# Kernel optimization log

Hardware: AMD Instinct MI355X
Metric: run time of the kernel (lower is better)

## Reference

```python
import jax, jax.numpy as jnp
import numpy as np

D_MODEL = 1024
N_HEADS = 16
D_K = D_MODEL // N_HEADS
D_FF = 4096
B, S = 2, 2048
EPS = 1e-5
SCALE = 0.02


def setup_inputs() -> dict:
    key = jax.random.key(0)
    ks = jax.random.split(key, 8)
    return {
        "x": jax.random.normal(ks[0], (B, S, D_MODEL), dtype=jnp.float32),
        "ln1_w": jnp.ones((D_MODEL,), jnp.float32),
        "ln1_b": jnp.zeros((D_MODEL,), jnp.float32),
        "Wq": jax.random.normal(ks[1], (D_MODEL, D_MODEL), jnp.float32) * SCALE,
        "bq": jnp.zeros((D_MODEL,), jnp.float32),
        "Wk": jax.random.normal(ks[2], (D_MODEL, D_MODEL), jnp.float32) * SCALE,
        "bk": jnp.zeros((D_MODEL,), jnp.float32),
        "Wv": jax.random.normal(ks[3], (D_MODEL, D_MODEL), jnp.float32) * SCALE,
        "bv": jnp.zeros((D_MODEL,), jnp.float32),
        "Wo": jax.random.normal(ks[4], (D_MODEL, D_MODEL), jnp.float32) * SCALE,
        "bo": jnp.zeros((D_MODEL,), jnp.float32),
        "ln2_w": jnp.ones((D_MODEL,), jnp.float32),
        "ln2_b": jnp.zeros((D_MODEL,), jnp.float32),
        "W1": jax.random.normal(ks[5], (D_MODEL, D_FF), jnp.float32) * SCALE,
        "b1": jnp.zeros((D_FF,), jnp.float32),
        "W2": jax.random.normal(ks[6], (D_FF, D_MODEL), jnp.float32) * SCALE,
        "b2": jnp.zeros((D_MODEL,), jnp.float32),
    }


def _layernorm(x, w, b):
    mu = jnp.mean(x, axis=-1, keepdims=True)
    var = jnp.mean(jnp.square(x - mu), axis=-1, keepdims=True)
    return (x - mu) * jax.lax.rsqrt(var + EPS) * w + b


def reference(x, ln1_w, ln1_b, Wq, bq, Wk, bk, Wv, bv, Wo, bo,
              ln2_w, ln2_b, W1, b1, W2, b2):
    # Pre-norm multi-head self-attention (dropout = identity, eval mode)
    h = _layernorm(x, ln1_w, ln1_b)                      # [B,S,D]
    q = (h @ Wq + bq).reshape(B, S, N_HEADS, D_K)        # [B,S,H,Dk]
    k = (h @ Wk + bk).reshape(B, S, N_HEADS, D_K)
    v = (h @ Wv + bv).reshape(B, S, N_HEADS, D_K)
    scores = jnp.einsum('bqhd,bkhd->bhqk', q, k) / jnp.sqrt(jnp.float32(D_K))
    attn = jax.nn.softmax(scores, axis=-1)               # [B,H,S,S]
    ctx = jnp.einsum('bhqk,bkhd->bqhd', attn, v).reshape(B, S, D_MODEL)
    x = x + (ctx @ Wo + bo)
    # Pre-norm FFN
    h2 = _layernorm(x, ln2_w, ln2_b)
    ff = jax.nn.relu(h2 @ W1 + b1) @ W2 + b2
    return x + ff
```

## Files before the change

kernel.cpp:

```cpp
#include <hip/hip_runtime.h>
#include <hip/hip_bf16.h>
#include <cstdint>
#include <cstddef>

typedef unsigned short ushort_t;
typedef __bf16 bf16x8 __attribute__((ext_vector_type(8)));
typedef float f32x4 __attribute__((ext_vector_type(4)));

#define D_MODEL 1024
#define D_FF 4096
#define BB 2
#define SS 2048
#define NH 16
#define MROWS (BB * SS)
#define KVBLK 64

__device__ __forceinline__ ushort_t f2bf(float f) {
  union { float f; unsigned u; } x; x.f = f;
  unsigned r = x.u + 0x7fffu + ((x.u >> 16) & 1u);
  return (ushort_t)(r >> 16);
}

__device__ __forceinline__ void gload_lds16(const void* g, void* l) {
  __builtin_amdgcn_global_load_lds((const __attribute__((address_space(1))) void*)g,
                                   (__attribute__((address_space(3))) void*)l, 16, 0, 0);
}

__device__ __forceinline__ float dpp_sum16(float x) {
  int v;
  v = __builtin_amdgcn_update_dpp(0, __float_as_int(x), 0xB1, 0xF, 0xF, true);
  x += __int_as_float(v);
  v = __builtin_amdgcn_update_dpp(0, __float_as_int(x), 0x4E, 0xF, 0xF, true);
  x += __int_as_float(v);
  v = __builtin_amdgcn_update_dpp(0, __float_as_int(x), 0x141, 0xF, 0xF, true);
  x += __int_as_float(v);
  v = __builtin_amdgcn_update_dpp(0, __float_as_int(x), 0x140, 0xF, 0xF, true);
  x += __int_as_float(v);
  return x;
}

__global__ __launch_bounds__(256) void ln_bf16_kernel(
    const float* __restrict__ x, const float* __restrict__ w,
    const float* __restrict__ b, ushort_t* __restrict__ out) {
  int row = blockIdx.x;
  int tid = threadIdx.x;
  int lane = tid & 63, wid = tid >> 6;
  const float4 v = ((const float4*)(x + (size_t)row * D_MODEL))[tid];
  float s = v.x + v.y + v.z + v.w;
  __shared__ float red[8];
  #pragma unroll
  for (int o = 32; o > 0; o >>= 1) s += __shfl_down(s, o);
  if (lane == 0) red[wid] = s;
  __syncthreads();
  float mu = (red[0] + red[1] + red[2] + red[3]) * (1.0f / D_MODEL);
  float d0 = v.x - mu, d1 = v.y - mu, d2 = v.z - mu, d3 = v.w - mu;
  float sq = d0 * d0 + d1 * d1 + d2 * d2 + d3 * d3;
  #pragma unroll
  for (int o = 32; o > 0; o >>= 1) sq += __shfl_down(sq, o);
  if (lane == 0) red[4 + wid] = sq;
  __syncthreads();
  float var = (red[4] + red[5] + red[6] + red[7]) * (1.0f / D_MODEL);
  float rstd = rsqrtf(var + 1e-5f);
  const float4 wv = ((const float4*)w)[tid];
  const float4 bv = ((const float4*)b)[tid];
  ushort4 o4;
  o4.x = f2bf(d0 * rstd * wv.x + bv.x);
  o4.y = f2bf(d1 * rstd * wv.y + bv.y);
  o4.z = f2bf(d2 * rstd * wv.z + bv.z);
  o4.w = f2bf(d3 * rstd * wv.w + bv.w);
  ((ushort4*)(out + (size_t)row * D_MODEL))[tid] = o4;
}

__global__ __launch_bounds__(256) void transpose_cast_kernel(
    const float* __restrict__ W, ushort_t* __restrict__ Wt, int K, int N) {
  __shared__ float tile[32][33];
  int bx = blockIdx.x * 32;
  int by = blockIdx.y * 32;
  int tx = threadIdx.x, ty = threadIdx.y;
  #pragma unroll
  for (int i = 0; i < 32; i += 8)
    tile[ty + i][tx] = W[(size_t)(by + ty + i) * N + bx + tx];
  __syncthreads();
  #pragma unroll
  for (int i = 0; i < 32; i += 8)
    Wt[(size_t)(bx + ty + i) * K + by + tx] = f2bf(tile[tx][ty + i]);
}

__global__ __launch_bounds__(256) void vtrans_kernel(
    const ushort_t* __restrict__ qkv, ushort_t* __restrict__ Vt) {
  __shared__ __align__(16) ushort_t T[64 * 64];
  const int tid = threadIdx.x;
  const int bh = blockIdx.y, b = bh >> 4, h = bh & 15;
  const int kv0 = blockIdx.x * 64;
  const ushort_t* Vp = qkv + (size_t)b * SS * 3072 + 2048 + h * 64;
  #pragma unroll
  for (int i = 0; i < 2; i++) {
    int idx = tid * 2 + i;
    int key = idx >> 3, c = idx & 7;
    bf16x8 v = *(const bf16x8*)(Vp + (size_t)(kv0 + key) * 3072 + c * 8);
    *(bf16x8*)(T + key * 64 + ((c ^ (key & 7)) * 8)) = v;
  }
  __syncthreads();
  int d = tid >> 2, kb = tid & 3;
  ushort_t o[16];
  #pragma unroll
  for (int j = 0; j < 16; j++) {
    int key = kb * 16 + j;
    o[j] = T[key * 64 + (((d >> 3) ^ (key & 7)) * 8) + (d & 7)];
  }
  ushort_t* dst = Vt + (size_t)(bh * 64 + d) * SS + kv0 + kb * 16;
  *(bf16x8*)dst = *(bf16x8*)&o[0];
  *(bf16x8*)(dst + 8) = *(bf16x8*)&o[8];
}

template <int EPI>
__global__ __launch_bounds__(256, 2) void gemm128_kernel(
    const ushort_t* __restrict__ A, const ushort_t* __restrict__ Bt,
    const float* __restrict__ bias, const float* __restrict__ resid,
    void* __restrict__ Cout, int M, int N, int K, int NTn) {
  __shared__ __align__(16) ushort_t lds[4][2][4096];
  const int tid = threadIdx.x, lane = tid & 63, wid = tid >> 6;
  const int wm = wid >> 1, wn = wid & 1;
  const int rl = lane & 15, cg = lane >> 4;
  int nwg = gridDim.x;
  int q = nwg >> 3, rr = nwg & 7;
  int xcd = blockIdx.x & 7, idx = blockIdx.x >> 3;
  int wgid = (xcd < rr ? xcd * (q + 1) : rr * (q + 1) + (xcd - rr) * q) + idx;
  const int row0 = (wgid / NTn) * 128, col0 = (wgid - (wgid / NTn) * NTn) * 128;
  const int NT = K / 32;

  int soff[2], ldso[2];
  #pragma unroll
  for (int i = 0; i < 2; i++) {
    int ci = wid * 128 + i * 64 + lane;
    int P = ci * 16;
    int L = P ^ (((P >> 7) & 7) << 4);
    int row = L >> 6, kc = (L >> 4) & 3;
    soff[i] = row * K + kc * 8;
    ldso[i] = (wid * 128 + i * 64) * 8;
  }

  f32x4 acc[4][4] = {};

  auto stage = [&](int t) {
    int b = t & 3;
    int kk = t * 32;
    #pragma unroll
    for (int i = 0; i < 2; i++) {
      gload_lds16(A + (size_t)row0 * K + kk + soff[i], &lds[b][0][ldso[i]]);
      gload_lds16(Bt + (size_t)col0 * K + kk + soff[i], &lds[b][1][ldso[i]]);
    }
  };

  auto compute = [&](int t) {
    int b = t & 3;
    bf16x8 af[4], bfv[4];
    #pragma unroll
    for (int mi = 0; mi < 4; mi++) {
      int r = wm * 64 + mi * 16 + rl;
      int L = r * 64 + cg * 16;
      int P = L ^ (((L >> 7) & 7) << 4);
      af[mi] = *(const bf16x8*)&lds[b][0][P >> 1];
    }
    #pragma unroll
    for (int ni = 0; ni < 4; ni++) {
      int r = wn * 64 + ni * 16 + rl;
      int L = r * 64 + cg * 16;
      int P = L ^ (((L >> 7) & 7) << 4);
      bfv[ni] = *(const bf16x8*)&lds[b][1][P >> 1];
    }
    __builtin_amdgcn_s_setprio(1);
    #pragma unroll
    for (int mi = 0; mi < 4; mi++)
      #pragma unroll
      for (int ni = 0; ni < 4; ni++)
        acc[mi][ni] = __builtin_amdgcn_mfma_f32_16x16x32_bf16(af[mi], bfv[ni], acc[mi][ni], 0, 0, 0);
    __builtin_amdgcn_s_setprio(0);
  };

  stage(0); stage(1); stage(2);
  for (int t = 0; t < NT; ++t) {
    if (t < NT - 2)       asm volatile("s_waitcnt vmcnt(8)" ::: "memory");
    else if (t == NT - 2) asm volatile("s_waitcnt vmcnt(4)" ::: "memory");
    else                  asm volatile("s_waitcnt vmcnt(0)" ::: "memory");
    __builtin_amdgcn_s_barrier();
    __builtin_amdgcn_sched_barrier(0);
    if (t + 3 < NT) stage(t + 3);
    compute(t);
  }

  if (EPI == 2) {
    float* out = (float*)Cout;
    #pragma unroll
    for (int ni = 0; ni < 4; ni++) {
      int col = col0 + wn * 64 + ni * 16 + rl;
      float bv = bias[col];
      #pragma unroll
      for (int mi = 0; mi < 4; mi++) {
        int rowb = row0 + wm * 64 + mi * 16 + cg * 4;
        #pragma unroll
        for (int j = 0; j < 4; j++)
          out[(size_t)(rowb + j) * N + col] =
              acc[mi][ni][j] + bv + resid[(size_t)(rowb + j) * N + col];
      }
    }
  } else {
    ushort_t* out = (ushort_t*)Cout;
    #pragma unroll
    for (int ni = 0; ni < 4; ni++) {
      int col = col0 + wn * 64 + ni * 16 + rl;
      float bv = bias[col];
      float sc = (EPI == 0 && col < 1024) ? 0.18033688011f : 1.0f;
      #pragma unroll
      for (int mi = 0; mi < 4; mi++) {
        int rowb = row0 + wm * 64 + mi * 16 + cg * 4;
        #pragma unroll
        for (int j = 0; j < 4; j++) {
          float v = acc[mi][ni][j] + bv;
          if (EPI == 1) v = fmaxf(v, 0.0f);
          if (EPI == 0) v *= sc;
          out[(size_t)(rowb + j) * N + col] = f2bf(v);
        }
      }
    }
  }
}

__global__ __launch_bounds__(256) void attn_kernel(
    const ushort_t* __restrict__ qkv, const ushort_t* __restrict__ Vt,
    ushort_t* __restrict__ ctx) {
  __shared__ __align__(16) ushort_t Kl[2][64 * 64];
  __shared__ __align__(16) ushort_t Vl[2][64 * 64];
  __shared__ __align__(16) ushort_t Pl[4][16 * 64];
  const int tid = threadIdx.x, lane = tid & 63, wid = tid >> 6;
  int bid = blockIdx.y * 32 + blockIdx.x;
  int w = (bid & 7) * 128 + (bid >> 3);
  const int bh = w >> 5, qt = w & 31;
  const int b = bh >> 4, h = bh & 15;
  const int q0 = qt * 64 + wid * 16;
  const ushort_t* Qp = qkv + (size_t)b * SS * 3072 + h * 64;
  const ushort_t* Kp = Qp + 1024;
  const ushort_t* Vg = Vt + (size_t)bh * 64 * SS;

  bf16x8 qf[2];
  {
    int qr = q0 + (lane & 15);
    #pragma unroll
    for (int s2 = 0; s2 < 2; s2++)
      qf[s2] = *(const bf16x8*)(Qp + (size_t)qr * 3072 + s2 * 32 + (lane >> 4) * 8);
  }
  float l[4];
  f32x4 acc[4] = {};
  #pragma unroll
  for (int r = 0; r < 4; r++) l[r] = 0.f;

  const int NT = SS / KVBLK;

  int ksrc[2], vsrc[2];
  #pragma unroll
  for (int i = 0; i < 2; i++) {
    int idx = wid * 128 + i * 64 + lane;
    int R = idx >> 3, c = idx & 7;
    int key = (R & 15) * 4 + (R >> 4);
    ksrc[i] = key * 3072 + ((c ^ (R & 7)) * 8);
    vsrc[i] = R * SS + ((c ^ (R & 7)) * 8);
  }
  const int ldsb = wid * 1024;

  auto stageKV = [&](int buf, int t) {
    size_t kvK = (size_t)t * KVBLK * 3072;
    int kvV = t * KVBLK;
    gload_lds16(Kp + kvK + ksrc[0], &Kl[buf][ldsb]);
    gload_lds16(Kp + kvK + ksrc[1], &Kl[buf][ldsb + 512]);
    gload_lds16(Vg + kvV + vsrc[0], &Vl[buf][ldsb]);
    gload_lds16(Vg + kvV + vsrc[1], &Vl[buf][ldsb + 512]);
  };

  auto body = [&](int t, int cb) {
    __syncthreads();
    if (t + 1 < NT) stageKV(cb ^ 1, t + 1);

    f32x4 s4[4] = {};
    #pragma unroll
    for (int g = 0; g < 4; g++) {
      const ushort_t* kr = &Kl[cb][(g * 16 + (lane & 15)) * 64];
      bf16x8 kf0 = *(const bf16x8*)(kr + (((lane >> 4)) ^ ((lane & 15) & 7)) * 8);
      bf16x8 kf1 = *(const bf16x8*)(kr + ((4 + (lane >> 4)) ^ ((lane & 15) & 7)) * 8);
      s4[g] = __builtin_amdgcn_mfma_f32_16x16x32_bf16(qf[0], kf0, s4[g], 0, 0, 0);
      s4[g] = __builtin_amdgcn_mfma_f32_16x16x32_bf16(qf[1], kf1, s4[g], 0, 0, 0);
    }
    const int qrow = (lane >> 4) * 4;
    const int cp = (lane & 15) >> 1, hf = (lane & 15) & 1;
    #pragma unroll
    for (int r = 0; r < 4; r++) {
      float p0 = __builtin_amdgcn_exp2f(s4[0][r]);
      float p1 = __builtin_amdgcn_exp2f(s4[1][r]);
      float p2 = __builtin_amdgcn_exp2f(s4[2][r]);
      float p3 = __builtin_amdgcn_exp2f(s4[3][r]);
      l[r] += (p0 + p1) + (p2 + p3);
      unsigned w0, w1;
      asm("v_cvt_pk_bf16_f32 %0, %1, %2" : "=v"(w0) : "v"(p0), "v"(p1));
      asm("v_cvt_pk_bf16_f32 %0, %1, %2" : "=v"(w1) : "v"(p2), "v"(p3));
      uint2 pw; pw.x = w0; pw.y = w1;
      int qq = qrow + r;
      *(uint2*)(&Pl[wid][qq * 64 + ((cp ^ (qq & 7)) * 8) + hf * 4]) = pw;
    }
    asm volatile("s_waitcnt lgkmcnt(0)" ::: "memory");
    __builtin_amdgcn_sched_barrier(0);
    bf16x8 pf[2];
    {
      int qq = lane & 15;
      #pragma unroll
      for (int ks = 0; ks < 2; ks++) {
        int c = ks * 4 + (lane >> 4);
        pf[ks] = *(const bf16x8*)(&Pl[wid][qq * 64 + ((c ^ (qq & 7)) * 8)]);
      }
    }
    #pragma unroll
    for (int f = 0; f < 4; f++) {
      int d = f * 16 + (lane & 15);
      #pragma unroll
      for (int ks = 0; ks < 2; ks++) {
        int chunk = (ks * 4 + (lane >> 4)) ^ (d & 7);
        bf16x8 vf = *(const bf16x8*)(&Vl[cb][d * 64 + chunk * 8]);
        acc[f] = __builtin_amdgcn_mfma_f32_16x16x32_bf16(pf[ks], vf, acc[f], 0, 0, 0);
      }
    }
  };

  stageKV(0, 0);
  for (int t = 0; t < NT; t += 2) {
    body(t, 0);
    body(t + 1, 1);
  }

  #pragma unroll
  for (int r = 0; r < 4; r++) l[r] = dpp_sum16(l[r]);
  float rl4[4];
  #pragma unroll
  for (int r = 0; r < 4; r++) rl4[r] = 1.0f / l[r];
  #pragma unroll
  for (int f = 0; f < 4; f++)
    #pragma unroll
    for (int r = 0; r < 4; r++) {
      int row = b * SS + q0 + (lane >> 4) * 4 + r;
      int col = h * 64 + f * 16 + (lane & 15);
      ctx[(size_t)row * D_MODEL + col] = f2bf(acc[f][r] * rl4[r]);
    }
}

extern "C" void kernel_launch(void* const* d_in, const int* in_sizes, int n_in,
                              void* d_out, int out_size, void* d_ws, size_t ws_size,
                              hipStream_t stream) {
  const float* x    = (const float*)d_in[0];
  const float* ln1w = (const float*)d_in[1];
  const float* ln1b = (const float*)d_in[2];
  const float* Wq   = (const float*)d_in[3];
  const float* bq   = (const float*)d_in[4];
  const float* Wk   = (const float*)d_in[5];
  const float* bk   = (const float*)d_in[6];
  const float* Wv   = (const float*)d_in[7];
  const float* bv   = (const float*)d_in[8];
  const float* Wo   = (const float*)d_in[9];
  const float* bo   = (const float*)d_in[10];
  const float* ln2w = (const float*)d_in[11];
  const float* ln2b = (const float*)d_in[12];
  const float* W1   = (const float*)d_in[13];
  const float* b1   = (const float*)d_in[14];
  const float* W2   = (const float*)d_in[15];
  const float* b2   = (const float*)d_in[16];

  char* ws = (char*)d_ws;
  size_t off = 0;
  auto alloc = [&](size_t bytes) {
    void* p = ws + off;
    off += (bytes + 255) & ~(size_t)255;
    return p;
  };
  ushort_t* Wt_qkv = (ushort_t*)alloc((size_t)3072 * 1024 * 2);
  ushort_t* Wt_o   = (ushort_t*)alloc((size_t)1024 * 1024 * 2);
  ushort_t* Wt_1   = (ushort_t*)alloc((size_t)4096 * 1024 * 2);
  ushort_t* Wt_2   = (ushort_t*)alloc((size_t)1024 * 4096 * 2);
  float*    bqkv   = (float*)alloc((size_t)3072 * 4);
  ushort_t* qkvb   = (ushort_t*)alloc((size_t)MROWS * 3072 * 2);
  ushort_t* ctxb   = (ushort_t*)alloc((size_t)MROWS * 1024 * 2);
  ushort_t* hbuf   = (ushort_t*)alloc((size_t)MROWS * 1024 * 2);
  float*    x2     = (float*)alloc((size_t)MROWS * 1024 * 4);
  ushort_t* Vtb    = (ushort_t*)alloc((size_t)BB * NH * 64 * SS * 2);
  ushort_t* ff1    = qkvb;
  float*    outp   = (float*)d_out;

  dim3 tb(32, 8);
  transpose_cast_kernel<<<dim3(32, 32), tb, 0, stream>>>(Wq, Wt_qkv, 1024, 1024);
  transpose_cast_kernel<<<dim3(32, 32), tb, 0, stream>>>(Wk, Wt_qkv + 1024 * 1024, 1024, 1024);
  transpose_cast_kernel<<<dim3(32, 32), tb, 0, stream>>>(Wv, Wt_qkv + 2 * 1024 * 1024, 1024, 1024);
  transpose_cast_kernel<<<dim3(32, 32), tb, 0, stream>>>(Wo, Wt_o, 1024, 1024);
  transpose_cast_kernel<<<dim3(128, 32), tb, 0, stream>>>(W1, Wt_1, 1024, 4096);
  transpose_cast_kernel<<<dim3(32, 128), tb, 0, stream>>>(W2, Wt_2, 4096, 1024);
  hipMemcpyAsync(bqkv,        bq, 1024 * 4, hipMemcpyDeviceToDevice, stream);
  hipMemcpyAsync(bqkv + 1024, bk, 1024 * 4, hipMemcpyDeviceToDevice, stream);
  hipMemcpyAsync(bqkv + 2048, bv, 1024 * 4, hipMemcpyDeviceToDevice, stream);

  ln_bf16_kernel<<<MROWS, 256, 0, stream>>>(x, ln1w, ln1b, hbuf);
  gemm128_kernel<0><<<dim3(24 * 32), 256, 0, stream>>>(
      hbuf, Wt_qkv, bqkv, nullptr, qkvb, MROWS, 3072, 1024, 24);
  vtrans_kernel<<<dim3(SS / 64, BB * NH), 256, 0, stream>>>(qkvb, Vtb);
  attn_kernel<<<dim3(SS / 64, BB * NH), 256, 0, stream>>>(qkvb, Vtb, ctxb);
  gemm128_kernel<2><<<dim3(8 * 32), 256, 0, stream>>>(
      ctxb, Wt_o, bo, x, x2, MROWS, 1024, 1024, 8);
  ln_bf16_kernel<<<MROWS, 256, 0, stream>>>(x2, ln2w, ln2b, hbuf);
  gemm128_kernel<1><<<dim3(32 * 32), 256, 0, stream>>>(
      hbuf, Wt_1, b1, nullptr, ff1, MROWS, D_FF, 1024, 32);
  gemm128_kernel<2><<<dim3(8 * 32), 256, 0, stream>>>(
      ff1, Wt_2, b2, x2, outp, MROWS, 1024, 4096, 8);
}
```

Baseline: 254.6 us.

## Add 64x128-tile GEMM kernel for N=1024 residual projections to fill more CUs

Adds a gemm64_kernel that uses 64x128 output tiles, 3-stage LDS buffering and an XCD-aware workgroup remap. It replaces the 128x128 gemm for the Wo and W2 projections (the N=1024 outputs with fp32 residual epilogue). This doubles the workgroup count from 256 to 512, giving better occupancy across the MI355X CUs. The cost is more redundant B-tile loads and smaller per-wave MFMA reuse.

Result: slower. 269.6 us (+5.9%).

```diff
diff --git a/kernel.cpp b/kernel.cpp
--- a/kernel.cpp
+++ b/kernel.cpp
@@ -189,39 +189,116 @@
     compute(t);
   }
 
-  if (EPI == 2) {
-    float* out = (float*)Cout;
+  ushort_t* out = (ushort_t*)Cout;
+  #pragma unroll
+  for (int ni = 0; ni < 4; ni++) {
+    int col = col0 + wn * 64 + ni * 16 + rl;
+    float bv = bias[col];
+    float sc = (EPI == 0 && col < 1024) ? 0.18033688011f : 1.0f;
+    #pragma unroll
+    for (int mi = 0; mi < 4; mi++) {
+      int rowb = row0 + wm * 64 + mi * 16 + cg * 4;
+      #pragma unroll
+      for (int j = 0; j < 4; j++) {
+        float v = acc[mi][ni][j] + bv;
+        if (EPI == 1) v = fmaxf(v, 0.0f);
+        if (EPI == 0) v *= sc;
+        out[(size_t)(rowb + j) * N + col] = f2bf(v);
+      }
+    }
+  }
+}
+
+__global__ __launch_bounds__(256, 4) void gemm64_kernel(
+    const ushort_t* __restrict__ A, const ushort_t* __restrict__ Bt,
+    const float* __restrict__ bias, const float* __restrict__ resid,
+    float* __restrict__ Cout, int M, int N, int K, int NTn) {
+  __shared__ __align__(16) ushort_t lA[3][2048];
+  __shared__ __align__(16) ushort_t lB[3][4096];
+  const int tid = threadIdx.x, lane = tid & 63, wid = tid >> 6;
+  const int wm = wid >> 1, wn = wid & 1;
+  const int rl = lane & 15, cg = lane >> 4;
+  int nwg = gridDim.x;
+  int q = nwg >> 3, rr = nwg & 7;
+  int xcd = blockIdx.x & 7, idx = blockIdx.x >> 3;
+  int wgid = (xcd < rr ? xcd * (q + 1) : rr * (q + 1) + (xcd - rr) * q) + idx;
+  const int row0 = (wgid / NTn) * 64, col0 = (wgid - (wgid / NTn) * NTn) * 128;
+  const int NT = K / 32;
+
+  int soffA, ldsoA, soffB[2], ldsoB[2];
+  {
+    int ci = wid * 64 + lane;
+    int P = ci * 16;
+    int L = P ^ (((P >> 7) & 7) << 4);
+    soffA = (L >> 6) * K + ((L >> 4) & 3) * 8;
+    ldsoA = wid * 512;
+  }
+  #pragma unroll
+  for (int i = 0; i < 2; i++) {
+    int ci = wid * 128 + i * 64 + lane;
+    int P = ci * 16;
+    int L = P ^ (((P >> 7) & 7) << 4);
+    soffB[i] = (L >> 6) * K + ((L >> 4) & 3) * 8;
+    ldsoB[i] = (wid * 128 + i * 64) * 8;
+  }
+
+  f32x4 acc[2][4] = {};
+
+  auto stage = [&](int t, int b) {
+    int kk = t * 32;
+    gload_lds16(A + (size_t)row0 * K + kk + soffA, &lA[b][ldsoA]);
+    gload_lds16(Bt + (size_t)col0 * K + kk + soffB[0], &lB[b][ldsoB[0]]);
+    gload_lds16(Bt + (size_t)col0 * K + kk + soffB[1], &lB[b][ldsoB[1]]);
+  };
+
+  auto compute = [&](int b) {
+    bf16x8 af[2], bfv[4];
+    #pragma unroll
+    for (int mi = 0; mi < 2; mi++) {
+      int r = wm * 32 + mi * 16 + rl;
+      int L = r * 64 + cg * 16;
+      int P = L ^ (((L >> 7) & 7) << 4);
+      af[mi] = *(const bf16x8*)&lA[b][P >> 1];
+    }
     #pragma unroll
     for (int ni = 0; ni < 4; ni++) {
-      int col = col0 + wn * 64 + ni * 16 + rl;
-      float bv = bias[col];
-      #pragma unroll
-      for (int mi = 0; mi < 4; mi++) {
-        int rowb = row0 + wm * 64 + mi * 16 + cg * 4;
-        #pragma unroll
-        for (int j = 0; j < 4; j++)
-          out[(size_t)(rowb + j) * N + col] =
-              acc[mi][ni][j] + bv + resid[(size_t)(rowb + j) * N + col];
-      }
-    }
-  } else {
-    ushort_t* out = (ushort_t*)Cout;
-    #pragma unroll
-    for (int ni = 0; ni < 4; ni++) {
-      int col = col0 + wn * 64 + ni * 16 + rl;
-      float bv = bias[col];
-      float sc = (EPI == 0 && col < 1024) ? 0.18033688011f : 1.0f;
-      #pragma unroll
-      for (int mi = 0; mi < 4; mi++) {
-        int rowb = row0 + wm * 64 + mi * 16 + cg * 4;
-        #pragma unroll
-        for (int j = 0; j < 4; j++) {
-          float v = acc[mi][ni][j] + bv;
-          if (EPI == 1) v = fmaxf(v, 0.0f);
-          if (EPI == 0) v *= sc;
-          out[(size_t)(rowb + j) * N + col] = f2bf(v);
-        }
-      }
+      int r = wn * 64 + ni * 16 + rl;
+      int L = r * 64 + cg * 16;
+      int P = L ^ (((L >> 7) & 7) << 4);
+      bfv[ni] = *(const bf16x8*)&lB[b][P >> 1];
+    }
+    __builtin_amdgcn_s_setprio(1);
+    #pragma unroll
+    for (int mi = 0; mi < 2; mi++)
+      #pragma unroll
+      for (int ni = 0; ni < 4; ni++)
+        acc[mi][ni] = __builtin_amdgcn_mfma_f32_16x16x32_bf16(af[mi], bfv[ni], acc[mi][ni], 0, 0, 0);
+    __builtin_amdgcn_s_setprio(0);
+  };
+
+  stage(0, 0); stage(1, 1);
+  int sb = 2, cb = 0;
+  for (int t = 0; t < NT; ++t) {
+    if (t < NT - 1) asm volatile("s_waitcnt vmcnt(3)" ::: "memory");
+    else            asm volatile("s_waitcnt vmcnt(0)" ::: "memory");
+    __builtin_amdgcn_s_barrier();
+    __builtin_amdgcn_sched_barrier(0);
+    if (t + 2 < NT) { stage(t + 2, sb); sb = (sb == 2) ? 0 : sb + 1; }
+    compute(cb);
+    cb = (cb == 2) ? 0 : cb + 1;
+  }
+
+  #pragma unroll
+  for (int ni = 0; ni < 4; ni++) {
+    int col = col0 + wn * 64 + ni * 16 + rl;
+    float bv = bias[col];
+    #pragma unroll
+    for (int mi = 0; mi < 2; mi++) {
+      int rowb = row0 + wm * 32 + mi * 16 + cg * 4;
+      #pragma unroll
+      for (int j = 0; j < 4; j++)
+        Cout[(size_t)(rowb + j) * N + col] =
+            acc[mi][ni][j] + bv + resid[(size_t)(rowb + j) * N + col];
     }
   }
 }
@@ -406,11 +483,11 @@
       hbuf, Wt_qkv, bqkv, nullptr, qkvb, MROWS, 3072, 1024, 24);
   vtrans_kernel<<<dim3(SS / 64, BB * NH), 256, 0, stream>>>(qkvb, Vtb);
   attn_kernel<<<dim3(SS / 64, BB * NH), 256, 0, stream>>>(qkvb, Vtb, ctxb);
-  gemm128_kernel<2><<<dim3(8 * 32), 256, 0, stream>>>(
+  gemm64_kernel<<<dim3(64 * 8), 256, 0, stream>>>(
       ctxb, Wt_o, bo, x, x2, MROWS, 1024, 1024, 8);
   ln_bf16_kernel<<<MROWS, 256, 0, stream>>>(x2, ln2w, ln2b, hbuf);
   gemm128_kernel<1><<<dim3(32 * 32), 256, 0, stream>>>(
       hbuf, Wt_1, b1, nullptr, ff1, MROWS, D_FF, 1024, 32);
-  gemm128_kernel<2><<<dim3(8 * 32), 256, 0, stream>>>(
+  gemm64_kernel<<<dim3(64 * 8), 256, 0, stream>>>(
       ff1, Wt_2, b2, x2, outp, MROWS, 1024, 4096, 8);
 }
```

## Split-K the W2 FFN GEMM into two partials plus a reduction kernel

Applied to the files above, without the earlier changes.

The final FFN down-projection (K=4096) only launched 256 workgroups, which underfills the GPU. It now splits K into two halves, launching 512 workgroups that write fp32 partials. A new reduce kernel sums the partials and adds bias and residual. This costs an extra 32MB partial write and a read pass plus one more launch, and it falls back to the old path when workspace is short.

Result: no change. 253.5 us (-0.4%).

```diff
diff --git a/kernel.cpp b/kernel.cpp
--- a/kernel.cpp
+++ b/kernel.cpp
@@ -117,7 +117,7 @@
 __global__ __launch_bounds__(256, 2) void gemm128_kernel(
     const ushort_t* __restrict__ A, const ushort_t* __restrict__ Bt,
     const float* __restrict__ bias, const float* __restrict__ resid,
-    void* __restrict__ Cout, int M, int N, int K, int NTn) {
+    void* __restrict__ Cout, int M, int N, int K, int NTn, int Ksplit, int MTN) {
   __shared__ __align__(16) ushort_t lds[4][2][4096];
   const int tid = threadIdx.x, lane = tid & 63, wid = tid >> 6;
   const int wm = wid >> 1, wn = wid & 1;
@@ -126,8 +126,11 @@
   int q = nwg >> 3, rr = nwg & 7;
   int xcd = blockIdx.x & 7, idx = blockIdx.x >> 3;
   int wgid = (xcd < rr ? xcd * (q + 1) : rr * (q + 1) + (xcd - rr) * q) + idx;
-  const int row0 = (wgid / NTn) * 128, col0 = (wgid - (wgid / NTn) * NTn) * 128;
-  const int NT = K / 32;
+  const int s = wgid / MTN;
+  int rem = wgid - s * MTN;
+  const int row0 = (rem / NTn) * 128, col0 = (rem - (rem / NTn) * NTn) * 128;
+  const int k0 = s * Ksplit;
+  const int NT = Ksplit / 32;
 
   int soff[2], ldso[2];
   #pragma unroll
@@ -144,7 +147,7 @@
 
   auto stage = [&](int t) {
     int b = t & 3;
-    int kk = t * 32;
+    int kk = k0 + t * 32;
     #pragma unroll
     for (int i = 0; i < 2; i++) {
       gload_lds16(A + (size_t)row0 * K + kk + soff[i], &lds[b][0][ldso[i]]);
@@ -202,6 +205,19 @@
         for (int j = 0; j < 4; j++)
           out[(size_t)(rowb + j) * N + col] =
               acc[mi][ni][j] + bv + resid[(size_t)(rowb + j) * N + col];
+      }
+    }
+  } else if (EPI == 3) {
+    float* out = (float*)Cout + (size_t)s * M * N;
+    #pragma unroll
+    for (int ni = 0; ni < 4; ni++) {
+      int col = col0 + wn * 64 + ni * 16 + rl;
+      #pragma unroll
+      for (int mi = 0; mi < 4; mi++) {
+        int rowb = row0 + wm * 64 + mi * 16 + cg * 4;
+        #pragma unroll
+        for (int j = 0; j < 4; j++)
+          out[(size_t)(rowb + j) * N + col] = acc[mi][ni][j];
       }
     }
   } else {
@@ -223,6 +239,27 @@
         }
       }
     }
+  }
+}
+
+__global__ __launch_bounds__(256) void reduce_kernel(
+    const float* __restrict__ p, const float* __restrict__ bias,
+    const float* __restrict__ resid, float* __restrict__ out,
+    int S, size_t total4, size_t stride4) {
+  const float4* p4 = (const float4*)p;
+  const float4* r4 = (const float4*)resid;
+  const float4* b4 = (const float4*)bias;
+  float4* o4 = (float4*)out;
+  for (size_t i = (size_t)blockIdx.x * 256 + threadIdx.x; i < total4;
+       i += (size_t)gridDim.x * 256) {
+    float4 a = r4[i];
+    float4 bb = b4[i & 255];
+    a.x += bb.x; a.y += bb.y; a.z += bb.z; a.w += bb.w;
+    for (int s = 0; s < S; ++s) {
+      float4 v = p4[(size_t)s * stride4 + i];
+      a.x += v.x; a.y += v.y; a.z += v.z; a.w += v.w;
+    }
+    o4[i] = a;
   }
 }
 
@@ -390,6 +427,10 @@
   ushort_t* ff1    = qkvb;
   float*    outp   = (float*)d_out;
 
+  const size_t partial1 = (size_t)MROWS * 1024 * 4;
+  int S = (ws_size - off >= 2 * partial1 + 256) ? 2 : 1;
+  float* pbuf = (S == 2) ? (float*)alloc(2 * partial1) : nullptr;
+
   dim3 tb(32, 8);
   transpose_cast_kernel<<<dim3(32, 32), tb, 0, stream>>>(Wq, Wt_qkv, 1024, 1024);
   transpose_cast_kernel<<<dim3(32, 32), tb, 0, stream>>>(Wk, Wt_qkv + 1024 * 1024, 1024, 1024);
@@ -403,14 +444,21 @@
 
   ln_bf16_kernel<<<MROWS, 256, 0, stream>>>(x, ln1w, ln1b, hbuf);
   gemm128_kernel<0><<<dim3(24 * 32), 256, 0, stream>>>(
-      hbuf, Wt_qkv, bqkv, nullptr, qkvb, MROWS, 3072, 1024, 24);
+      hbuf, Wt_qkv, bqkv, nullptr, qkvb, MROWS, 3072, 1024, 24, 1024, 24 * 32);
   vtrans_kernel<<<dim3(SS / 64, BB * NH), 256, 0, stream>>>(qkvb, Vtb);
   attn_kernel<<<dim3(SS / 64, BB * NH), 256, 0, stream>>>(qkvb, Vtb, ctxb);
   gemm128_kernel<2><<<dim3(8 * 32), 256, 0, stream>>>(
-      ctxb, Wt_o, bo, x, x2, MROWS, 1024, 1024, 8);
+      ctxb, Wt_o, bo, x, x2, MROWS, 1024, 1024, 8, 1024, 8 * 32);
   ln_bf16_kernel<<<MROWS, 256, 0, stream>>>(x2, ln2w, ln2b, hbuf);
   gemm128_kernel<1><<<dim3(32 * 32), 256, 0, stream>>>(
-      hbuf, Wt_1, b1, nullptr, ff1, MROWS, D_FF, 1024, 32);
-  gemm128_kernel<2><<<dim3(8 * 32), 256, 0, stream>>>(
-      ff1, Wt_2, b2, x2, outp, MROWS, 1024, 4096, 8);
-}
+      hbuf, Wt_1, b1, nullptr, ff1, MROWS, D_FF, 1024, 32, 1024, 32 * 32);
+  if (S == 2) {
+    gemm128_kernel<3><<<dim3(8 * 32 * 2), 256, 0, stream>>>(
+        ff1, Wt_2, nullptr, nullptr, pbuf, MROWS, 1024, 4096, 8, 2048, 8 * 32);
+    reduce_kernel<<<2048, 256, 0, stream>>>(pbuf, b2, x2, outp, 2,
+        (size_t)MROWS * 1024 / 4, (size_t)MROWS * 1024 / 4);
+  } else {
+    gemm128_kernel<2><<<dim3(8 * 32), 256, 0, stream>>>(
+        ff1, Wt_2, b2, x2, outp, MROWS, 1024, 4096, 8, 4096, 8 * 32);
+  }
+}
```
